# Kernel optimization log

Measured on AMD Instinct MI355X. Metric: run time of the kernel, lower is better.

Reference implementation:

```python
import jax, jax.numpy as jnp
import numpy as np

IN_CH, OUT_CH = 32, 32
MODES1, MODES2 = 16, 16
B, L, H, W = 8, 16, 64, 33


def setup_inputs() -> dict:
    key = jax.random.key(0)
    k = jax.random.split(key, 6)
    scale = 1.0 / (IN_CH * OUT_CH)
    wshape = (IN_CH, OUT_CH, MODES1, MODES2)
    return {
        "x_re": jax.random.normal(k[0], (B, L, IN_CH, H, W), dtype=jnp.float32),
        "x_im": jax.random.normal(k[1], (B, L, IN_CH, H, W), dtype=jnp.float32),
        "w1_re": scale * jax.random.normal(k[2], wshape, dtype=jnp.float32),
        "w1_im": scale * jax.random.normal(k[3], wshape, dtype=jnp.float32),
        "w2_re": scale * jax.random.normal(k[4], wshape, dtype=jnp.float32),
        "w2_im": scale * jax.random.normal(k[5], wshape, dtype=jnp.float32),
    }


def _mul2d(x, w):
    # x: [B, L, C_in, m1, m2] complex; w: [C_in, C_out, m1, m2] complex
    return jnp.einsum("blcij,coij->bloij", x, w)


def reference(x_re, x_im, w1_re, w1_im, w2_re, w2_im):
    x = jax.lax.complex(x_re, x_im)          # [B, L, C, H, W] complex64
    w1 = jax.lax.complex(w1_re, w1_im)       # [C_in, C_out, m1, m2]
    w2 = jax.lax.complex(w2_re, w2_im)
    Bx, Lx, Cx, Hx, Wx = x.shape
    m1 = min(Hx, MODES1)
    m2 = min(Wx, MODES2)

    out = jnp.zeros((Bx, Lx, OUT_CH, Hx, Wx), dtype=x.dtype)
    # low positive frequencies (top-left corner)
    out = out.at[:, :, :, :m1, :m2].set(
        _mul2d(x[:, :, :, :m1, :m2], w1[:, :, :m1, :m2]))
    # low negative frequencies along H (bottom-left corner)
    if Hx > 1 and (Hx > MODES1 or Wx > MODES2):
        out = out.at[:, :, :, -m1:, :m2].set(
            _mul2d(x[:, :, :, -m1:, :m2], w2[:, :, :m1, :m2]))
    # return complex result as trailing real/imag dim (float32)
    return jnp.stack([out.real, out.imag], axis=-1)
```

## Files before the change

### kernel.cpp

```cpp
#include <hip/hip_runtime.h>

#define IN_CH 32
#define OUT_CH 32
#define M1 16
#define M2 16
#define H_ 64
#define W_ 33
#define HW (H_*W_)
#define BLPB 8
#define WSTRIDE (OUT_CH*M1*M2)

__global__ __launch_bounds__(256) void fill_zero(float* __restrict__ out) {
    const int tid = blockIdx.x * 256 + threadIdx.x;
    const int nthreads = gridDim.x * 256;

    float4* out4 = (float4*)out;
    const float4 z4 = make_float4(0.f, 0.f, 0.f, 0.f);
    const int totalA = 4096 * 528;
    for (int idx = tid; idx < totalA; idx += nthreads) {
        int plane = idx / 528;
        int k = idx - plane * 528;
        out4[(long)plane * 1056 + 264 + k] = z4;
    }

    float2* out2 = (float2*)out;
    const float2 z2 = make_float2(0.f, 0.f);
    const int totalB = 4096 * 32 * 17;
    for (int idx = tid; idx < totalB; idx += nthreads) {
        int plane = idx / 544;
        int r = idx - plane * 544;
        int hh = r / 17;
        int t = r - hh * 17;
        int h = hh < 16 ? hh : hh + 32;
        out2[(long)plane * 2112 + h * 33 + 16 + t] = z2;
    }
}

__global__ __launch_bounds__(256) void spectral_compute(
    const float* __restrict__ x_re, const float* __restrict__ x_im,
    const float* __restrict__ w1_re, const float* __restrict__ w1_im,
    const float* __restrict__ w2_re, const float* __restrict__ w2_im,
    float* __restrict__ out)
{
    const int tid = threadIdx.x;
    const int blk = blockIdx.x;
    const int chunk = blk & 15;
    const int ri = blk >> 4;
    const int region = ri >> 4;
    const int i = ri & 15;
    const int h = region ? (48 + i) : i;
    const int bl0 = chunk * BLPB;

    __shared__ float2 xs[BLPB][IN_CH][M2];

    for (int item = tid; item < BLPB * IN_CH * M2; item += 256) {
        int j = item & 15;
        int c = (item >> 4) & 31;
        int b = item >> 9;
        long src = (long)((bl0 + b) * IN_CH + c) * HW + (long)h * W_ + j;
        xs[b][c][j] = make_float2(x_re[src], x_im[src]);
    }
    __syncthreads();

    const int j  = tid & 15;
    const int o0 = tid >> 4;
    const float* __restrict__ wre = region ? w2_re : w1_re;
    const float* __restrict__ wim = region ? w2_im : w1_im;

    float2 acc0[BLPB], acc1[BLPB];
    #pragma unroll
    for (int b = 0; b < BLPB; ++b) {
        acc0[b] = make_float2(0.f, 0.f);
        acc1[b] = make_float2(0.f, 0.f);
    }

    const int wbase = (o0 * M1 + i) * M2 + j;
    #pragma unroll 4
    for (int c = 0; c < IN_CH; ++c) {
        int idx = wbase + c * WSTRIDE;
        float wr0 = wre[idx],        wi0 = wim[idx];
        float wr1 = wre[idx + 4096], wi1 = wim[idx + 4096];
        #pragma unroll
        for (int b = 0; b < BLPB; ++b) {
            float2 xc = xs[b][c][j];
            acc0[b].x = fmaf(xc.x, wr0, acc0[b].x); acc0[b].x = fmaf(-xc.y, wi0, acc0[b].x);
            acc0[b].y = fmaf(xc.x, wi0, acc0[b].y); acc0[b].y = fmaf( xc.y, wr0, acc0[b].y);
            acc1[b].x = fmaf(xc.x, wr1, acc1[b].x); acc1[b].x = fmaf(-xc.y, wi1, acc1[b].x);
            acc1[b].y = fmaf(xc.x, wi1, acc1[b].y); acc1[b].y = fmaf( xc.y, wr1, acc1[b].y);
        }
    }

    float2* out2 = (float2*)out;
    #pragma unroll
    for (int b = 0; b < BLPB; ++b) {
        long plane = (long)(bl0 + b) * OUT_CH;
        long d0 = (plane + o0)      * HW + (long)h * W_ + j;
        long d1 = (plane + o0 + 16) * HW + (long)h * W_ + j;
        out2[d0] = acc0[b];
        out2[d1] = acc1[b];
    }
}

extern "C" void kernel_launch(void* const* d_in, const int* in_sizes, int n_in,
                              void* d_out, int out_size, void* d_ws, size_t ws_size,
                              hipStream_t stream) {
    const float* x_re  = (const float*)d_in[0];
    const float* x_im  = (const float*)d_in[1];
    const float* w1_re = (const float*)d_in[2];
    const float* w1_im = (const float*)d_in[3];
    const float* w2_re = (const float*)d_in[4];
    const float* w2_im = (const float*)d_in[5];
    float* out = (float*)d_out;

    fill_zero<<<dim3(2048), dim3(256), 0, stream>>>(out);
    spectral_compute<<<dim3(512), dim3(256), 0, stream>>>(
        x_re, x_im, w1_re, w1_im, w2_re, w2_im, out);
}
```

Baseline: 40.05 us.

## Fuse zero-fill and spectral compute into one interleaved kernel launch

```diff
diff --git a/kernel.cpp b/kernel.cpp
--- a/kernel.cpp
+++ b/kernel.cpp
@@ -7,45 +7,47 @@
 #define H_ 64
 #define W_ 33
 #define HW (H_*W_)
-#define BLPB 8
+#define BLPB 4
 #define WSTRIDE (OUT_CH*M1*M2)
 
-__global__ __launch_bounds__(256) void fill_zero(float* __restrict__ out) {
-    const int tid = blockIdx.x * 256 + threadIdx.x;
-    const int nthreads = gridDim.x * 256;
-
-    float4* out4 = (float4*)out;
-    const float4 z4 = make_float4(0.f, 0.f, 0.f, 0.f);
-    const int totalA = 4096 * 528;
-    for (int idx = tid; idx < totalA; idx += nthreads) {
-        int plane = idx / 528;
-        int k = idx - plane * 528;
-        out4[(long)plane * 1056 + 264 + k] = z4;
-    }
-
-    float2* out2 = (float2*)out;
-    const float2 z2 = make_float2(0.f, 0.f);
-    const int totalB = 4096 * 32 * 17;
-    for (int idx = tid; idx < totalB; idx += nthreads) {
-        int plane = idx / 544;
-        int r = idx - plane * 544;
-        int hh = r / 17;
-        int t = r - hh * 17;
-        int h = hh < 16 ? hh : hh + 32;
-        out2[(long)plane * 2112 + h * 33 + 16 + t] = z2;
-    }
-}
-
-__global__ __launch_bounds__(256) void spectral_compute(
+__global__ __launch_bounds__(256) void spectral_fused(
     const float* __restrict__ x_re, const float* __restrict__ x_im,
     const float* __restrict__ w1_re, const float* __restrict__ w1_im,
     const float* __restrict__ w2_re, const float* __restrict__ w2_im,
     float* __restrict__ out)
 {
     const int tid = threadIdx.x;
-    const int blk = blockIdx.x;
-    const int chunk = blk & 15;
-    const int ri = blk >> 4;
+
+    if (blockIdx.x & 1) {
+        const int fid = blockIdx.x >> 1;
+        const int gtid = fid * 256 + tid;
+        const int nthreads = 1024 * 256;
+
+        float4* out4 = (float4*)out;
+        const float4 z4 = make_float4(0.f, 0.f, 0.f, 0.f);
+        const int totalA = 4096 * 528;
+        for (int idx = gtid; idx < totalA; idx += nthreads) {
+            int plane = idx / 528;
+            int k = idx - plane * 528;
+            out4[(long)plane * 1056 + 264 + k] = z4;
+        }
+        float2* out2 = (float2*)out;
+        const float2 z2 = make_float2(0.f, 0.f);
+        const int totalB = 4096 * 544;
+        for (int idx = gtid; idx < totalB; idx += nthreads) {
+            int plane = idx / 544;
+            int r = idx - plane * 544;
+            int hh = r / 17;
+            int t = r - hh * 17;
+            int h = hh < 16 ? hh : hh + 32;
+            out2[(long)plane * 2112 + h * 33 + 16 + t] = z2;
+        }
+        return;
+    }
+
+    const int cid = blockIdx.x >> 1;
+    const int ri = cid >> 5;
+    const int chunk = cid & 31;
     const int region = ri >> 4;
     const int i = ri & 15;
     const int h = region ? (48 + i) : i;
@@ -64,8 +66,8 @@
 
     const int j  = tid & 15;
     const int o0 = tid >> 4;
-    const float* __restrict__ wre = region ? w2_re : w1_re;
-    const float* __restrict__ wim = region ? w2_im : w1_im;
+    const float* __restrict__ wre = (region ? w2_re : w1_re) + (o0 * M1 + i) * M2 + j;
+    const float* __restrict__ wim = (region ? w2_im : w1_im) + (o0 * M1 + i) * M2 + j;
 
     float2 acc0[BLPB], acc1[BLPB];
     #pragma unroll
@@ -74,10 +76,9 @@
         acc1[b] = make_float2(0.f, 0.f);
     }
 
-    const int wbase = (o0 * M1 + i) * M2 + j;
-    #pragma unroll 4
+    #pragma unroll 8
     for (int c = 0; c < IN_CH; ++c) {
-        int idx = wbase + c * WSTRIDE;
+        int idx = c * WSTRIDE;
         float wr0 = wre[idx],        wi0 = wim[idx];
         float wr1 = wre[idx + 4096], wi1 = wim[idx + 4096];
         #pragma unroll
@@ -112,7 +113,6 @@
     const float* w2_im = (const float*)d_in[5];
     float* out = (float*)d_out;
 
-    fill_zero<<<dim3(2048), dim3(256), 0, stream>>>(out);
-    spectral_compute<<<dim3(512), dim3(256), 0, stream>>>(
+    spectral_fused<<<dim3(2048), dim3(256), 0, stream>>>(
         x_re, x_im, w1_re, w1_im, w2_re, w2_im, out);
 }
```

Result: faster. 37.83 us (-5.5%).
